# Performance work log

Measured on AMD Instinct MI355X. Metric: run time of the kernel, lower is better.

The kernel has to match this reference:

```python
import jax, jax.numpy as jnp
import numpy as np

NUM_CODES = 8192
CODE_DIM = 256
DECAY = 0.99
EPSILON = 1e-05
COMMITMENT_COST = 0.25


def setup_inputs() -> dict:
    key = jax.random.key(0)
    kz, ke = jax.random.split(key)
    z = jax.random.normal(kz, (8, 4096, CODE_DIM), dtype=jnp.float32)
    emb = jax.random.normal(ke, (NUM_CODES, CODE_DIM), dtype=jnp.float32)
    emb = emb / jnp.linalg.norm(emb, axis=1, keepdims=True)
    return {
        "z": z,
        "embedding": emb,
        "ema_cluster_size": jnp.zeros((NUM_CODES,), dtype=jnp.float32),
        "ema_embedding": emb,
    }


def reference(z, embedding, ema_cluster_size, ema_embedding):
    K, D = embedding.shape
    z_flat = z.reshape(-1, D)  # [N, D]
    # squared euclidean distances: [N, K]
    distances = (
        jnp.sum(z_flat * z_flat, axis=1, keepdims=True)
        - 2.0 * z_flat @ embedding.T
        + jnp.sum(embedding * embedding, axis=1)
    )
    indices = jnp.argmin(distances, axis=1)  # [N]
    z_q = embedding[indices]  # [N, D]

    # EMA update (training path); segment_sum replaces one-hot matmul scatter
    cluster_size = jax.ops.segment_sum(
        jnp.ones((z_flat.shape[0],), dtype=z_flat.dtype), indices, num_segments=K
    )
    new_ema_cluster_size = ema_cluster_size * DECAY + cluster_size * (1.0 - DECAY)
    dw = jax.ops.segment_sum(z_flat, indices, num_segments=K)  # [K, D]
    new_ema_embedding = ema_embedding * DECAY + dw * (1.0 - DECAY)
    n = jnp.sum(new_ema_cluster_size)
    smoothed = (new_ema_cluster_size + EPSILON) / (n + K * EPSILON) * n
    new_embedding = new_ema_embedding / smoothed[:, None]

    # straight-through (torch: z_q + (z_flat - z_q).detach())
    z_q_st = z_q + jax.lax.stop_gradient(z_flat - z_q)
    vq_loss = COMMITMENT_COST * jnp.mean((jax.lax.stop_gradient(z_q) - z_flat) ** 2)

    z_q_st = z_q_st.reshape(z.shape)
    indices = indices.reshape(z.shape[:-1])
    return (z_q_st, indices, vq_loss, new_embedding, new_ema_cluster_size, new_ema_embedding)
```

## Files before the change

### kernel.cpp

```cpp
#include <hip/hip_runtime.h>

#define NPTS   32768
#define NCODES 8192
#define DIM    256

#define DECAYF 0.99f
#define ONE_MINUS_DECAYF ((float)(1.0 - 0.99))
#define EPSF   1e-5f
#define KEPSF  ((float)(8192.0 * 1e-5))
#define MARGIN 0.05f

#define WS_PART  0
#define WS_A     (WS_PART + NPTS / 4 * 8)
#define WS_EN    (WS_A + NPTS * 4)
#define WS_CNT   (WS_EN + NCODES * 4)
#define WS_S     (WS_CNT + NCODES * 4)
#define WS_IDX   (WS_S + NCODES * 4)
#define WS_OFFS  (WS_IDX + NPTS * 4)
#define WS_CUR   (WS_OFFS + NCODES * 4)
#define WS_PLIST (WS_CUR + NCODES * 4)
#define WS_EMBT  (WS_PLIST + NPTS * 4)
#define WS_GMIN  (WS_EMBT + (size_t)DIM * NCODES * 4)
#define WS_AH    (WS_GMIN + (size_t)NPTS * 512 * 4)
#define WS_BH    (WS_AH + (size_t)NPTS * DIM * 2)

typedef __attribute__((ext_vector_type(8))) short short8;
typedef __attribute__((ext_vector_type(4))) float f32x4;

__device__ inline void gl_lds16(const void* g, void* l) {
    __builtin_amdgcn_global_load_lds(
        (const __attribute__((address_space(1))) void*)g,
        (__attribute__((address_space(3))) void*)l, 16, 0, 0);
}

__device__ inline unsigned short f2bf(float f) {
    unsigned u = __float_as_uint(f);
    return (unsigned short)((u + 0x7FFFu + ((u >> 16) & 1u)) >> 16);
}
__device__ inline unsigned f2ord(float f) {
    unsigned u = __float_as_uint(f);
    return (u & 0x80000000u) ? ~u : (u | 0x80000000u);
}

__global__ __launch_bounds__(256) void k_prep0(int* __restrict__ cnt) {
    int i = blockIdx.x * blockDim.x + threadIdx.x;
    if (i < NCODES) cnt[i] = 0;
}

__global__ __launch_bounds__(256) void k_rownorm(const float* __restrict__ x,
                                                 float* __restrict__ outn,
                                                 int nrows) {
    int w = (blockIdx.x * blockDim.x + threadIdx.x) >> 6;
    int lane = threadIdx.x & 63;
    if (w >= nrows) return;
    const float4 v = *(const float4*)(x + (size_t)w * DIM + 4 * lane);
    float q0 = v.x * v.x, q1 = v.y * v.y, q2 = v.z * v.z, q3 = v.w * v.w;
    double s = (double)q0 + (double)q1 + (double)q2 + (double)q3;
    #pragma unroll
    for (int off = 32; off > 0; off >>= 1) s += __shfl_down(s, off);
    if (lane == 0) outn[w] = (float)s;
}

__global__ __launch_bounds__(256) void k_split(const float* __restrict__ x,
                                               unsigned short* __restrict__ dst,
                                               int nelem) {
    int i = blockIdx.x * blockDim.x + threadIdx.x;
    int stride = gridDim.x * blockDim.x;
    for (int j = i; j < nelem; j += stride)
        dst[j] = f2bf(x[j]);
}

__global__ __launch_bounds__(256) void k_gemm_argmin(
    const unsigned short* __restrict__ Ah,
    const unsigned short* __restrict__ Bh,
    const float* __restrict__ en,
    float* __restrict__ gmin) {
    __shared__ __align__(16) unsigned short SBUF[16384];

    const int t = threadIdx.x;
    const int w = t >> 6, l = t & 63;
    const int quad = l >> 4, l15 = l & 15;
    const int wr = w >> 1, wc = w & 1;
    const int mb = blockIdx.x >> 6, nb = blockIdx.x & 63;
    const int mBase = mb * 128, nBase = nb * 128;

    const int xr = (t & 7) ^ ((t >> 3) & 7);
    const int rrow = t >> 3;
    const unsigned short* ag[4];
    const unsigned short* bg[4];
    #pragma unroll
    for (int i = 0; i < 4; ++i) {
        ag[i] = Ah + (size_t)(mBase + i * 32 + rrow) * DIM + xr * 8;
        bg[i] = Bh + (size_t)(nBase + i * 32 + rrow) * DIM + xr * 8;
    }

    f32x4 acc[4][4];
    #pragma unroll
    for (int i = 0; i < 4; ++i)
        #pragma unroll
        for (int j = 0; j < 4; ++j)
            acc[i][j] = (f32x4){0.f, 0.f, 0.f, 0.f};

    for (int kt = 0; kt < 4; ++kt) {
        __syncthreads();
        #pragma unroll
        for (int i = 0; i < 4; ++i) {
            gl_lds16(ag[i], &SBUF[(i * 256 + w * 64) * 8]);
            gl_lds16(bg[i], &SBUF[8192 + (i * 256 + w * 64) * 8]);
            ag[i] += 64; bg[i] += 64;
        }
        __syncthreads();
        #pragma unroll
        for (int kk = 0; kk < 2; ++kk) {
            const int kc = kk * 4 + quad;
            short8 a[4], b[4];
            #pragma unroll
            for (int ti = 0; ti < 4; ++ti) {
                int m = wr * 64 + ti * 16 + l15;
                a[ti] = *(const short8*)&SBUF[(m * 8 + (kc ^ (m & 7))) * 8];
                int n = wc * 64 + ti * 16 + l15;
                b[ti] = *(const short8*)&SBUF[8192 + (n * 8 + (kc ^ (n & 7))) * 8];
            }
            #pragma unroll
            for (int ti = 0; ti < 4; ++ti)
                #pragma unroll
                for (int tj = 0; tj < 4; ++tj)
                    acc[ti][tj] = __builtin_amdgcn_mfma_f32_16x16x32_bf16(
                        a[ti], b[tj], acc[ti][tj], 0, 0, 0);
        }
    }

    float enc[4];
    #pragma unroll
    for (int tj = 0; tj < 4; ++tj)
        enc[tj] = en[nBase + wc * 64 + tj * 16 + l15];

    __syncthreads();
    float* ov = (float*)SBUF;
    #pragma unroll
    for (int ti = 0; ti < 4; ++ti) {
        #pragma unroll
        for (int r = 0; r < 4; ++r) {
            float dmin = enc[0] - 2.0f * acc[ti][0][r];
            #pragma unroll
            for (int tj = 1; tj < 4; ++tj)
                dmin = fminf(dmin, enc[tj] - 2.0f * acc[ti][tj][r]);
            int p = wr * 64 + ti * 16 + quad * 4 + r;
            ov[(wc * 128 + p) * 16 + l15] = dmin;
        }
    }
    __syncthreads();
    #pragma unroll
    for (int it = 0; it < 4; ++it) {
        int id = it * 256 + t;
        int sg = id & 3;
        const float4 v = *(const float4*)&ov[(id >> 2) * 16 + sg * 4];
        float m = fminf(fminf(v.x, v.y), fminf(v.z, v.w));
        int pp = (id >> 2) & 127;
        int wcc = id >> 9;
        gmin[(size_t)(mBase + pp) * 512 + nb * 8 + wcc * 4 + sg] = m;
    }
}

__global__ __launch_bounds__(256) void k_phase2(
    const float* __restrict__ z, const float* __restrict__ emb,
    const float* __restrict__ A, const float* __restrict__ en,
    const float* __restrict__ gmin,
    int* __restrict__ widx, float* __restrict__ out1,
    int* __restrict__ cnt) {
    int wpt = (blockIdx.x << 2) + (threadIdx.x >> 6);
    int l = threadIdx.x & 63;

    const float* gp = gmin + (size_t)wpt * 512;
    float loc[8];
    #pragma unroll
    for (int i = 0; i < 8; ++i) loc[i] = gp[i * 64 + l];
    float m8 = loc[0];
    #pragma unroll
    for (int i = 1; i < 8; ++i) m8 = fminf(m8, loc[i]);
    #pragma unroll
    for (int off = 1; off < 64; off <<= 1) m8 = fminf(m8, __shfl_xor(m8, off));
    const float thresh = m8 + MARGIN;

    const float4 z4 = *(const float4*)(z + (size_t)wpt * DIM + 4 * l);
    const float Azn = A[wpt];
    unsigned long long best = ~0ull;
    #pragma unroll 1
    for (int i = 0; i < 8; ++i) {
        unsigned long long mask = __ballot(loc[i] <= thresh);
        while (mask) {
            int s = __ffsll((long long)mask) - 1;
            mask &= mask - 1;
            int gid = i * 64 + s;
            int cbase = (gid >> 3) * 128 + ((gid >> 2) & 1) * 64 + (gid & 3) * 4;
            #pragma unroll 4
            for (int k = 0; k < 16; ++k) {
                int c = cbase + (k >> 2) * 16 + (k & 3);
                const float4 ev = *(const float4*)(emb + (size_t)c * DIM + 4 * l);
                float p = fmaf(z4.x, ev.x,
                          fmaf(z4.y, ev.y,
                          fmaf(z4.z, ev.z, z4.w * ev.w)));
                #pragma unroll
                for (int off = 1; off < 64; off <<= 1) p += __shfl_xor(p, off);
                float dist = (Azn - 2.0f * p) + en[c];
                unsigned long long pk =
                    ((unsigned long long)f2ord(dist) << 32) | (unsigned)c;
                best = pk < best ? pk : best;
            }
        }
    }
    if (l == 0) {
        int idx = (int)(unsigned)best;
        widx[wpt] = idx;
        out1[wpt] = (float)idx;
        atomicAdd(cnt + idx, 1);
    }
}

__global__ __launch_bounds__(256) void k_scan(const int* __restrict__ cnt,
                                              const float* __restrict__ ecs,
                                              int* __restrict__ offs,
                                              int* __restrict__ cursor,
                                              float* __restrict__ out4,
                                              float* __restrict__ s_out) {
    __shared__ int ps[256];
    __shared__ double rd[256];
    __shared__ float nsh;
    int t = threadIdx.x;
    int base = t * 32;
    int loc[32];
    int s = 0;
    double nl = 0.0;
    #pragma unroll
    for (int i = 0; i < 32; ++i) {
        int c = cnt[base + i];
        loc[i] = c;
        s += c;
        float f = ecs[base + i] * DECAYF + (float)c * ONE_MINUS_DECAYF;
        out4[base + i] = f;
        nl += (double)f;
    }
    ps[t] = s;
    rd[t] = nl;
    __syncthreads();
    for (int off = 1; off < 256; off <<= 1) {
        int v = (t >= off) ? ps[t - off] : 0;
        __syncthreads();
        ps[t] += v;
        __syncthreads();
    }
    for (int off = 128; off > 0; off >>= 1) {
        if (t < off) rd[t] += rd[t + off];
        __syncthreads();
    }
    if (t == 0) nsh = (float)rd[0];
    __syncthreads();
    int run = (t == 0) ? 0 : ps[t - 1];
    #pragma unroll
    for (int i = 0; i < 32; ++i) {
        offs[base + i] = run;
        cursor[base + i] = run;
        run += loc[i];
    }
    float n = nsh;
    for (int k = t; k < NCODES; k += 256)
        s_out[k] = (out4[k] + EPSF) / (n + KEPSF) * n;
}

__global__ __launch_bounds__(256) void k_place(const int* __restrict__ widx,
                                               int* __restrict__ cursor,
                                               int* __restrict__ plist) {
    int p = blockIdx.x * 256 + threadIdx.x;
    int idx = widx[p];
    int slot = atomicAdd(&cursor[idx], 1);
    plist[slot] = p;
}

__global__ __launch_bounds__(256) void k_zq(const float* __restrict__ z,
                                            const float* __restrict__ emb,
                                            const int* __restrict__ widx,
                                            float* __restrict__ out0,
                                            double* __restrict__ part) {
    __shared__ double sred[4];
    int w = (blockIdx.x * blockDim.x + threadIdx.x) >> 6;
    int wv = threadIdx.x >> 6;
    int lane = threadIdx.x & 63;
    int idx = widx[w];
    const float4 zv = *(const float4*)(z + (size_t)w * DIM + 4 * lane);
    const float4 ev = *(const float4*)(emb + (size_t)idx * DIM + 4 * lane);

    float4 o;
    o.x = ev.x + (zv.x - ev.x);
    o.y = ev.y + (zv.y - ev.y);
    o.z = ev.z + (zv.z - ev.z);
    o.w = ev.w + (zv.w - ev.w);
    *(float4*)(out0 + (size_t)w * DIM + 4 * lane) = o;

    float t0 = ev.x - zv.x, t1 = ev.y - zv.y, t2 = ev.z - zv.z, t3 = ev.w - zv.w;
    float s0 = t0 * t0, s1 = t1 * t1, s2 = t2 * t2, s3 = t3 * t3;
    double ls = (double)s0 + (double)s1 + (double)s2 + (double)s3;
    #pragma unroll
    for (int off = 32; off > 0; off >>= 1) ls += __shfl_down(ls, off);
    if (lane == 0) sred[wv] = ls;
    __syncthreads();
    if (threadIdx.x == 0)
        part[blockIdx.x] = (sred[0] + sred[1]) + (sred[2] + sred[3]);
}

__global__ __launch_bounds__(256) void k_loss(const double* __restrict__ part,
                                              float* __restrict__ out2) {
    __shared__ double red[256];
    int t = threadIdx.x;
    double s = 0.0;
    for (int i = t; i < NPTS / 4; i += 256) s += part[i];
    red[t] = s;
    __syncthreads();
    for (int off = 128; off > 0; off >>= 1) {
        if (t < off) red[t] += red[t + off];
        __syncthreads();
    }
    if (t == 0)
        out2[0] = 0.25f * (float)(red[0] / (double)((size_t)NPTS * DIM));
}

__global__ __launch_bounds__(256) void k_dw(const float* __restrict__ z,
                                            const float* __restrict__ eem,
                                            const int* __restrict__ offs,
                                            const int* __restrict__ cnt,
                                            const int* __restrict__ plist,
                                            float* __restrict__ out5) {
    int c = blockIdx.x * 4 + (threadIdx.x >> 6);
    int lane = threadIdx.x & 63;
    int beg = offs[c], num = cnt[c];
    float4 acc = make_float4(0.f, 0.f, 0.f, 0.f);
    for (int j = 0; j < num; ++j) {
        int p = plist[beg + j];
        const float4 v = *(const float4*)(z + (size_t)p * DIM + 4 * lane);
        acc.x += v.x; acc.y += v.y; acc.z += v.z; acc.w += v.w;
    }
    const float4 e = *(const float4*)(eem + (size_t)c * DIM + 4 * lane);
    float4 o;
    o.x = e.x * DECAYF + acc.x * ONE_MINUS_DECAYF;
    o.y = e.y * DECAYF + acc.y * ONE_MINUS_DECAYF;
    o.z = e.z * DECAYF + acc.z * ONE_MINUS_DECAYF;
    o.w = e.w * DECAYF + acc.w * ONE_MINUS_DECAYF;
    *(float4*)(out5 + (size_t)c * DIM + 4 * lane) = o;
}

__global__ __launch_bounds__(256) void k_final(const float* __restrict__ out5,
                                               const float* __restrict__ s,
                                               float* __restrict__ out3) {
    int i = blockIdx.x * blockDim.x + threadIdx.x;
    int stride = gridDim.x * blockDim.x;
    for (int j = i; j < NCODES * DIM; j += stride)
        out3[j] = out5[j] / s[j >> 8];
}

extern "C" void kernel_launch(void* const* d_in, const int* in_sizes, int n_in,
                              void* d_out, int out_size, void* d_ws, size_t ws_size,
                              hipStream_t stream) {
    const float* z   = (const float*)d_in[0];
    const float* emb = (const float*)d_in[1];
    const float* ecs = (const float*)d_in[2];
    const float* eem = (const float*)d_in[3];

    float* out = (float*)d_out;
    float* out0 = out;
    float* out1 = out + 8388608;
    float* out2 = out + 8421376;
    float* out3 = out + 8421377;
    float* out4 = out + 10518529;
    float* out5 = out + 10526721;

    char* ws = (char*)d_ws;
    double* wPart = (double*)(ws + WS_PART);
    float*  wA    = (float*)(ws + WS_A);
    float*  wEn   = (float*)(ws + WS_EN);
    int*    wCnt  = (int*)(ws + WS_CNT);
    float*  wS    = (float*)(ws + WS_S);
    int*    wIdx  = (int*)(ws + WS_IDX);
    int*    wOffs = (int*)(ws + WS_OFFS);
    int*    wCur  = (int*)(ws + WS_CUR);
    int*    wPl   = (int*)(ws + WS_PLIST);
    float*  wGmin = (float*)(ws + WS_GMIN);
    unsigned short* wAh = (unsigned short*)(ws + WS_AH);
    unsigned short* wBh = (unsigned short*)(ws + WS_BH);

    hipLaunchKernelGGL(k_prep0, dim3(32), dim3(256), 0, stream, wCnt);
    hipLaunchKernelGGL(k_rownorm, dim3(NPTS / 4), dim3(256), 0, stream, z, wA, NPTS);
    hipLaunchKernelGGL(k_rownorm, dim3(NCODES / 4), dim3(256), 0, stream, emb, wEn, NCODES);
    hipLaunchKernelGGL(k_split, dim3(4096), dim3(256), 0, stream, z, wAh, NPTS * DIM);
    hipLaunchKernelGGL(k_split, dim3(1024), dim3(256), 0, stream, emb, wBh, NCODES * DIM);
    hipLaunchKernelGGL(k_gemm_argmin, dim3((NPTS / 128) * (NCODES / 128)), dim3(256), 0, stream,
                       wAh, wBh, wEn, wGmin);
    hipLaunchKernelGGL(k_phase2, dim3(NPTS / 4), dim3(256), 0, stream,
                       z, emb, wA, wEn, wGmin, wIdx, out1, wCnt);
    hipLaunchKernelGGL(k_scan, dim3(1), dim3(256), 0, stream,
                       wCnt, ecs, wOffs, wCur, out4, wS);
    hipLaunchKernelGGL(k_place, dim3(NPTS / 256), dim3(256), 0, stream, wIdx, wCur, wPl);
    hipLaunchKernelGGL(k_zq, dim3(NPTS / 4), dim3(256), 0, stream, z, emb, wIdx, out0, wPart);
    hipLaunchKernelGGL(k_loss, dim3(1), dim3(256), 0, stream, wPart, out2);
    hipLaunchKernelGGL(k_dw, dim3(NCODES / 4), dim3(256), 0, stream,
                       z, eem, wOffs, wCnt, wPl, out5);
    hipLaunchKernelGGL(k_final, dim3(2048), dim3(256), 0, stream, out5, wS, out3);
}
```

Before: 384.9 us.

## Rewrite GEMM-argmin as 256x256 double-buffered 8-wave pipelined MFMA kernel

Replaces the 128x128 single-buffered bf16 GEMM tile with a 256x256 tile on 512 threads. Global-to-LDS loads are split into quarter stages and double-buffered, interleaved with MFMA phases using barriers, setprio and explicit waitcnt. Codes become the M dimension, so the per-group minimum over 16 contiguous codes is reduced with shuffles, and phase2's candidate code mapping is updated to match. This aims to overlap memory with compute and raise arithmetic intensity, at the cost of much higher register and LDS pressure (128KB LDS per block).

```diff
diff --git a/kernel.cpp b/kernel.cpp
--- a/kernel.cpp
+++ b/kernel.cpp
@@ -70,95 +70,187 @@
         dst[j] = f2bf(x[j]);
 }
 
-__global__ __launch_bounds__(256) void k_gemm_argmin(
+__global__ __launch_bounds__(512, 2) void k_gemm_argmin(
+    const unsigned short* __restrict__ Ah,
+    const unsigned short* __restrict__ Bh,
+    const float* __restrict__ en,
+    float* __restrict__ gmin);
+
+template<int MH>
+__device__ __forceinline__ void dsr_a(const unsigned short* LB, int wr, int l15,
+                                      int l7, int quad, short8 (&af)[4][2]) {
+#pragma unroll
+    for (int m4 = 0; m4 < 4; ++m4) {
+        const int r = wr * 128 + (MH * 4 + m4) * 16 + l15;
+#pragma unroll
+        for (int kk = 0; kk < 2; ++kk)
+            af[m4][kk] = *(const short8*)&LB[(r * 8 + ((kk * 4 + quad) ^ l7)) * 8];
+    }
+}
+template<int NH>
+__device__ __forceinline__ void dsr_b(const unsigned short* LB, int wc, int l15,
+                                      int l7, int quad, short8 (&bf)[2][2]) {
+#pragma unroll
+    for (int n2 = 0; n2 < 2; ++n2) {
+        const int r = wc * 64 + (NH * 2 + n2) * 16 + l15;
+#pragma unroll
+        for (int kk = 0; kk < 2; ++kk)
+            bf[n2][kk] = *(const short8*)&LB[16384 + (r * 8 + ((kk * 4 + quad) ^ l7)) * 8];
+    }
+}
+template<int MH, int NH>
+__device__ __forceinline__ void mma8(const short8 (&af)[4][2], const short8 (&bf)[2][2],
+                                     f32x4 (&acc)[8][4]) {
+#pragma unroll
+    for (int m4 = 0; m4 < 4; ++m4)
+#pragma unroll
+        for (int n2 = 0; n2 < 2; ++n2)
+#pragma unroll
+            for (int kk = 0; kk < 2; ++kk)
+                acc[MH * 4 + m4][NH * 2 + n2] = __builtin_amdgcn_mfma_f32_16x16x32_bf16(
+                    af[m4][kk], bf[n2][kk], acc[MH * 4 + m4][NH * 2 + n2], 0, 0, 0);
+}
+
+__global__ __launch_bounds__(512, 2) void k_gemm_argmin(
     const unsigned short* __restrict__ Ah,
     const unsigned short* __restrict__ Bh,
     const float* __restrict__ en,
     float* __restrict__ gmin) {
-    __shared__ __align__(16) unsigned short SBUF[16384];
+    __shared__ __align__(16) unsigned short LDS[65536];
 
     const int t = threadIdx.x;
     const int w = t >> 6, l = t & 63;
-    const int quad = l >> 4, l15 = l & 15;
-    const int wr = w >> 1, wc = w & 1;
-    const int mb = blockIdx.x >> 6, nb = blockIdx.x & 63;
-    const int mBase = mb * 128, nBase = nb * 128;
-
-    const int xr = (t & 7) ^ ((t >> 3) & 7);
-    const int rrow = t >> 3;
-    const unsigned short* ag[4];
-    const unsigned short* bg[4];
-    #pragma unroll
-    for (int i = 0; i < 4; ++i) {
-        ag[i] = Ah + (size_t)(mBase + i * 32 + rrow) * DIM + xr * 8;
-        bg[i] = Bh + (size_t)(nBase + i * 32 + rrow) * DIM + xr * 8;
-    }
-
-    f32x4 acc[4][4];
-    #pragma unroll
-    for (int i = 0; i < 4; ++i)
-        #pragma unroll
-        for (int j = 0; j < 4; ++j)
-            acc[i][j] = (f32x4){0.f, 0.f, 0.f, 0.f};
-
+    const int quad = l >> 4, l15 = l & 15, l7 = l & 7;
+    const int wr = w >> 2, wc = w & 3;
+    const int cb = blockIdx.x & 31, pb = blockIdx.x >> 5;
+    const int cBase = cb * 256, pBase = pb * 256;
+
+    const int lrs0 = t >> 3;
+    const int xg = (t & 7) ^ (lrs0 & 7);
+    const int rA0s0 = lrs0;
+    const int rA0s1 = 128 + lrs0;
+    const int rB0s0 = (lrs0 & 31) | ((lrs0 >> 5) << 6);
+    const int rB0s1 = 128 + rB0s0;
+
+    const unsigned short* gA0s0 = Bh + (size_t)(cBase + rA0s0) * DIM + xg * 8;
+    const unsigned short* gA0s1 = Bh + (size_t)(cBase + rA0s1) * DIM + xg * 8;
+    const unsigned short* gB0s0 = Ah + (size_t)(pBase + rB0s0) * DIM + xg * 8;
+    const unsigned short* gB0s1 = Ah + (size_t)(pBase + rB0s1) * DIM + xg * 8;
+
+    const int dA0s0 = (w * 8) * 64;
+    const int dA0s1 = (128 + w * 8) * 64;
+    const int dB0s0 = (((w & 3) * 8) | ((w >> 2) << 6)) * 64;
+    const int dB0s1 = dB0s0 + 128 * 64;
+
+#define STG_A0(KT, BUFS) do { \
+        gl_lds16(gA0s0 + (KT) * 64, &LDS[(BUFS) + dA0s0]); \
+        gl_lds16(gA0s1 + (KT) * 64, &LDS[(BUFS) + dA0s1]); } while (0)
+#define STG_A1(KT, BUFS) do { \
+        gl_lds16(gA0s0 + 64 * DIM + (KT) * 64, &LDS[(BUFS) + dA0s0 + 64 * 64]); \
+        gl_lds16(gA0s1 + 64 * DIM + (KT) * 64, &LDS[(BUFS) + dA0s1 + 64 * 64]); } while (0)
+#define STG_B0(KT, BUFS) do { \
+        gl_lds16(gB0s0 + (KT) * 64, &LDS[(BUFS) + 16384 + dB0s0]); \
+        gl_lds16(gB0s1 + (KT) * 64, &LDS[(BUFS) + 16384 + dB0s1]); } while (0)
+#define STG_B1(KT, BUFS) do { \
+        gl_lds16(gB0s0 + 32 * DIM + (KT) * 64, &LDS[(BUFS) + 16384 + dB0s0 + 32 * 64]); \
+        gl_lds16(gB0s1 + 32 * DIM + (KT) * 64, &LDS[(BUFS) + 16384 + dB0s1 + 32 * 64]); } while (0)
+
+    f32x4 acc[8][4];
+#pragma unroll
+    for (int i = 0; i < 8; ++i)
+#pragma unroll
+        for (int j = 0; j < 4; ++j) acc[i][j] = (f32x4){0.f, 0.f, 0.f, 0.f};
+
+    STG_A0(0, 0); STG_B0(0, 0); STG_A1(0, 0); STG_B1(0, 0);
+    STG_A0(1, 32768); STG_B0(1, 32768);
+    asm volatile("s_waitcnt vmcnt(4)");
+    __builtin_amdgcn_sched_barrier(0);
+    __builtin_amdgcn_s_barrier();
+
+    short8 af[4][2], bf0[2][2], bf1[2][2];
+#pragma unroll
     for (int kt = 0; kt < 4; ++kt) {
-        __syncthreads();
-        #pragma unroll
-        for (int i = 0; i < 4; ++i) {
-            gl_lds16(ag[i], &SBUF[(i * 256 + w * 64) * 8]);
-            gl_lds16(bg[i], &SBUF[8192 + (i * 256 + w * 64) * 8]);
-            ag[i] += 64; bg[i] += 64;
+        const unsigned short* LB = &LDS[(kt & 1) << 15];
+        const int cbufS = (kt & 1) << 15;
+        const int obufS = cbufS ^ 32768;
+        dsr_a<0>(LB, wr, l15, l7, quad, af);
+        dsr_b<0>(LB, wc, l15, l7, quad, bf0);
+        if (kt + 1 < 4) STG_A1(kt + 1, obufS);
+        __builtin_amdgcn_s_barrier();
+        asm volatile("s_waitcnt lgkmcnt(0)");
+        __builtin_amdgcn_sched_barrier(0);
+        __builtin_amdgcn_s_setprio(1);
+        mma8<0, 0>(af, bf0, acc);
+        __builtin_amdgcn_s_setprio(0);
+        __builtin_amdgcn_s_barrier();
+        dsr_b<1>(LB, wc, l15, l7, quad, bf1);
+        if (kt + 1 < 4) STG_B1(kt + 1, obufS);
+        __builtin_amdgcn_s_barrier();
+        asm volatile("s_waitcnt lgkmcnt(0)");
+        __builtin_amdgcn_sched_barrier(0);
+        __builtin_amdgcn_s_setprio(1);
+        mma8<0, 1>(af, bf1, acc);
+        __builtin_amdgcn_s_setprio(0);
+        __builtin_amdgcn_s_barrier();
+        dsr_a<1>(LB, wr, l15, l7, quad, af);
+        if (kt + 2 < 4) STG_A0(kt + 2, cbufS);
+        __builtin_amdgcn_s_barrier();
+        asm volatile("s_waitcnt lgkmcnt(0)");
+        __builtin_amdgcn_sched_barrier(0);
+        __builtin_amdgcn_s_setprio(1);
+        mma8<1, 0>(af, bf0, acc);
+        __builtin_amdgcn_s_setprio(0);
+        __builtin_amdgcn_s_barrier();
+        if (kt + 2 < 4) STG_B0(kt + 2, cbufS);
+        __builtin_amdgcn_s_barrier();
+        __builtin_amdgcn_s_setprio(1);
+        mma8<1, 1>(af, bf1, acc);
+        __builtin_amdgcn_s_setprio(0);
+        if (kt < 2) {
+            asm volatile("s_waitcnt vmcnt(4)");
+            __builtin_amdgcn_sched_barrier(0);
+        } else if (kt == 2) {
+            asm volatile("s_waitcnt vmcnt(0)");
+            __builtin_amdgcn_sched_barrier(0);
         }
-        __syncthreads();
-        #pragma unroll
-        for (int kk = 0; kk < 2; ++kk) {
-            const int kc = kk * 4 + quad;
-            short8 a[4], b[4];
-            #pragma unroll
-            for (int ti = 0; ti < 4; ++ti) {
-                int m = wr * 64 + ti * 16 + l15;
-                a[ti] = *(const short8*)&SBUF[(m * 8 + (kc ^ (m & 7))) * 8];
-                int n = wc * 64 + ti * 16 + l15;
-                b[ti] = *(const short8*)&SBUF[8192 + (n * 8 + (kc ^ (n & 7))) * 8];
-            }
-            #pragma unroll
-            for (int ti = 0; ti < 4; ++ti)
-                #pragma unroll
-                for (int tj = 0; tj < 4; ++tj)
-                    acc[ti][tj] = __builtin_amdgcn_mfma_f32_16x16x32_bf16(
-                        a[ti], b[tj], acc[ti][tj], 0, 0, 0);
+        __builtin_amdgcn_s_barrier();
+    }
+#undef STG_A0
+#undef STG_A1
+#undef STG_B0
+#undef STG_B1
+
+    float* outl = (float*)LDS;
+#pragma unroll
+    for (int m = 0; m < 8; ++m) {
+        const float4 en4 = *(const float4*)&en[cBase + wr * 128 + m * 16 + quad * 4];
+#pragma unroll
+        for (int n = 0; n < 4; ++n) {
+            f32x4 a = acc[m][n];
+            float d0 = fmaf(-2.f, a[0], en4.x);
+            float d1 = fmaf(-2.f, a[1], en4.y);
+            float d2 = fmaf(-2.f, a[2], en4.z);
+            float d3 = fmaf(-2.f, a[3], en4.w);
+            float dm = fminf(fminf(d0, d1), fminf(d2, d3));
+            dm = fminf(dm, __shfl_xor(dm, 16));
+            dm = fminf(dm, __shfl_xor(dm, 32));
+            if (quad == 0)
+                outl[(wr * 8 + m) * 256 + wc * 64 + n * 16 + l15] = dm;
         }
     }
-
-    float enc[4];
-    #pragma unroll
-    for (int tj = 0; tj < 4; ++tj)
-        enc[tj] = en[nBase + wc * 64 + tj * 16 + l15];
-
     __syncthreads();
-    float* ov = (float*)SBUF;
-    #pragma unroll
-    for (int ti = 0; ti < 4; ++ti) {
-        #pragma unroll
-        for (int r = 0; r < 4; ++r) {
-            float dmin = enc[0] - 2.0f * acc[ti][0][r];
-            #pragma unroll
-            for (int tj = 1; tj < 4; ++tj)
-                dmin = fminf(dmin, enc[tj] - 2.0f * acc[ti][tj][r]);
-            int p = wr * 64 + ti * 16 + quad * 4 + r;
-            ov[(wc * 128 + p) * 16 + l15] = dmin;
+    {
+        const int pt = t >> 1, h = t & 1;
+#pragma unroll
+        for (int q2 = 0; q2 < 2; ++q2) {
+            const int g0 = (h * 2 + q2) * 4;
+            float4 v;
+            v.x = outl[(g0 + 0) * 256 + pt];
+            v.y = outl[(g0 + 1) * 256 + pt];
+            v.z = outl[(g0 + 2) * 256 + pt];
+            v.w = outl[(g0 + 3) * 256 + pt];
+            *(float4*)&gmin[(size_t)(pBase + pt) * 512 + cb * 16 + g0] = v;
         }
-    }
-    __syncthreads();
-    #pragma unroll
-    for (int it = 0; it < 4; ++it) {
-        int id = it * 256 + t;
-        int sg = id & 3;
-        const float4 v = *(const float4*)&ov[(id >> 2) * 16 + sg * 4];
-        float m = fminf(fminf(v.x, v.y), fminf(v.z, v.w));
-        int pp = (id >> 2) & 127;
-        int wcc = id >> 9;
-        gmin[(size_t)(mBase + pp) * 512 + nb * 8 + wcc * 4 + sg] = m;
     }
 }
 
@@ -191,11 +283,10 @@
         while (mask) {
             int s = __ffsll((long long)mask) - 1;
             mask &= mask - 1;
-            int gid = i * 64 + s;
-            int cbase = (gid >> 3) * 128 + ((gid >> 2) & 1) * 64 + (gid & 3) * 4;
+            int cbase = (i * 64 + s) << 4;
             #pragma unroll 4
             for (int k = 0; k < 16; ++k) {
-                int c = cbase + (k >> 2) * 16 + (k & 3);
+                int c = cbase + k;
                 const float4 ev = *(const float4*)(emb + (size_t)c * DIM + 4 * l);
                 float p = fmaf(z4.x, ev.x,
                           fmaf(z4.y, ev.y,
@@ -391,7 +482,7 @@
     hipLaunchKernelGGL(k_rownorm, dim3(NCODES / 4), dim3(256), 0, stream, emb, wEn, NCODES);
     hipLaunchKernelGGL(k_split, dim3(4096), dim3(256), 0, stream, z, wAh, NPTS * DIM);
     hipLaunchKernelGGL(k_split, dim3(1024), dim3(256), 0, stream, emb, wBh, NCODES * DIM);
-    hipLaunchKernelGGL(k_gemm_argmin, dim3((NPTS / 128) * (NCODES / 128)), dim3(256), 0, stream,
+    hipLaunchKernelGGL(k_gemm_argmin, dim3((NPTS / 256) * (NCODES / 256)), dim3(512), 0, stream,
                        wAh, wBh, wEn, wGmin);
     hipLaunchKernelGGL(k_phase2, dim3(NPTS / 4), dim3(256), 0, stream,
                        z, emb, wA, wEn, wGmin, wIdx, out1, wCnt);
```

New measurement: 415.9 us. 8.1% more time.
